# Performance work log

Hardware: AMD Instinct MI355X
Metric: run time of the kernel (lower is better)

## Reference

```python
import jax, jax.numpy as jnp
import numpy as np
from jax import lax

CHUNK = 256  # query chunk size (manual tiling block)

def setup_inputs() -> dict:
    key = jax.random.key(0)
    kq, kk, kv = jax.random.split(key, 3)
    shape = (2, 16, 2048, 128)  # [B, H, S, D]
    q = jax.random.normal(kq, shape, dtype=jnp.float32)
    k = jax.random.normal(kk, shape, dtype=jnp.float32)
    v = jax.random.normal(kv, shape, dtype=jnp.float32)
    return {"q": q, "k": k, "v": v}

def reference(q, k, v):
    # Chunked (memory-efficient) exact attention: softmax(QK^T/sqrt(D)) V,
    # computed one query block at a time so the full [S,S] score matrix
    # is never materialized.
    B, H, S, D = q.shape
    scale = jnp.asarray(1.0 / np.sqrt(D), dtype=q.dtype)
    n_chunks = S // CHUNK
    # [n_chunks, B, H, CHUNK, D]
    q_blocks = q.reshape(B, H, n_chunks, CHUNK, D).transpose(2, 0, 1, 3, 4)

    def step(carry, q_blk):
        # scores for this query block vs all keys: [B, H, CHUNK, S]
        s = jnp.einsum('bhqd,bhkd->bhqk', q_blk, k) * scale
        p = jax.nn.softmax(s, axis=-1)
        o = jnp.einsum('bhqk,bhkd->bhqd', p, v)
        return carry, o

    _, out_blocks = lax.scan(step, None, q_blocks)
    # [n_chunks, B, H, CHUNK, D] -> [B, H, S, D]
    out = out_blocks.transpose(1, 2, 0, 3, 4).reshape(B, H, S, D)
    return out
```

## Files before the change

kernel.cpp:

```cpp
#include <hip/hip_runtime.h>
#include <hip/hip_bf16.h>


typedef short short8 __attribute__((ext_vector_type(8)));
typedef float f32x4 __attribute__((ext_vector_type(4)));

#define MFMA16(a, b, c) __builtin_amdgcn_mfma_f32_16x16x32_bf16((a), (b), (c), 0, 0, 0)

#if __has_builtin(__builtin_amdgcn_exp2f)
#define EXP2(x) __builtin_amdgcn_exp2f(x)
#else
#define EXP2(x) exp2f(x)
#endif

constexpr int Dh  = 128;
constexpr int S_  = 2048;
constexpr int KVB = 64;
constexpr int NT  = S_ / KVB;
constexpr int WAVES = 8;
constexpr int QBLK  = 128;

__device__ __forceinline__ short f2bf(float f) {
    union { float f; unsigned u; } x; x.f = f;
    unsigned r = x.u + 0x7fffu + ((x.u >> 16) & 1u);
    return (short)(r >> 16);
}

__device__ __forceinline__ void gload16(const void* g, void* l) {
    __builtin_amdgcn_global_load_lds(
        (const __attribute__((address_space(1))) unsigned int*)g,
        (__attribute__((address_space(3))) unsigned int*)l, 16, 0, 0);
}

__global__ __launch_bounds__(256) void prep_k(const float* __restrict__ K,
                                              short* __restrict__ Kz) {
    int idx = blockIdx.x * 256 + threadIdx.x;
    int b   = idx & 15;
    int s   = (idx >> 4) & (S_ - 1);
    int sb  = b ^ (s & 15);
    const float* src = K + (size_t)(idx >> 4) * Dh + sb * 8;
    float4 f0 = ((const float4*)src)[0];
    float4 f1 = ((const float4*)src)[1];
    short8 o;
    o[0] = f2bf(f0.x); o[1] = f2bf(f0.y); o[2] = f2bf(f0.z); o[3] = f2bf(f0.w);
    o[4] = f2bf(f1.x); o[5] = f2bf(f1.y); o[6] = f2bf(f1.z); o[7] = f2bf(f1.w);
    *(short8*)(Kz + (size_t)idx * 8) = o;
}

__global__ __launch_bounds__(256) void prep_v(const float* __restrict__ V,
                                              short* __restrict__ Vt) {
    __shared__ short tr[64][72];
    int bid = blockIdx.x;
    int dg = bid & 1, seg = (bid >> 1) & 31, bh = bid >> 6;
    int t = threadIdx.x;
    int s = t >> 2, d0 = (t & 3) * 16;
    const float* src = V + (size_t)(bh * S_ + seg * 64 + s) * Dh + dg * 64 + d0;
    #pragma unroll
    for (int i = 0; i < 16; i += 4) {
        float4 f = *(const float4*)(src + i);
        tr[d0 + i + 0][s] = f2bf(f.x); tr[d0 + i + 1][s] = f2bf(f.y);
        tr[d0 + i + 2][s] = f2bf(f.z); tr[d0 + i + 3][s] = f2bf(f.w);
    }
    __syncthreads();
    int d = t >> 2, j0 = (t & 3) * 2;
    size_t ob = ((size_t)(bh * 32 + seg) * 128 + dg * 64 + d) * 64;
    #pragma unroll
    for (int jj = 0; jj < 2; ++jj) {
        int j = j0 + jj;
        int sj = (j ^ (d & 7)) * 8;
        short8 val = *(const short8*)&tr[d][sj];
        *(short8*)(Vt + ob + j * 8) = val;
    }
}

__global__ __launch_bounds__(512, 4)
void mea_fwd3(const float* __restrict__ Qg, const short* __restrict__ Kz,
              const short* __restrict__ Vt, float* __restrict__ Og, int nqt) {
    __shared__ __align__(16) short k0[KVB * Dh], k1[KVB * Dh];
    __shared__ __align__(16) short v0[Dh * KVB], v1[Dh * KVB];
    __shared__ __align__(16) short p_lds[WAVES][16][64];

    const int bid  = blockIdx.x;
    const int swz  = (bid & 7) * ((int)gridDim.x >> 3) + (bid >> 3);
    const int qt   = swz % nqt;
    const int bh   = swz / nqt;
    const int tid  = threadIdx.x;
    const int w    = tid >> 6;
    const int lane = tid & 63;
    const int lr   = lane & 15;
    const int lg   = lane >> 4;

    const size_t base  = (size_t)bh * S_ * Dh;
    const int    qrow0 = qt * QBLK + w * 16;
    const float  QSC = 0.08838834764831845f * 1.4426950408889634f;

    short8 qf[4];
    {
        const float* qp = Qg + base + (size_t)(qrow0 + lr) * Dh;
        #pragma unroll
        for (int kc = 0; kc < 4; ++kc) {
            const float4 f0 = *(const float4*)(qp + kc * 32 + lg * 8);
            const float4 f1 = *(const float4*)(qp + kc * 32 + lg * 8 + 4);
            short8 a;
            a[0] = f2bf(f0.x * QSC); a[1] = f2bf(f0.y * QSC);
            a[2] = f2bf(f0.z * QSC); a[3] = f2bf(f0.w * QSC);
            a[4] = f2bf(f1.x * QSC); a[5] = f2bf(f1.y * QSC);
            a[6] = f2bf(f1.z * QSC); a[7] = f2bf(f1.w * QSC);
            qf[kc] = a;
        }
    }

    f32x4 oacc[8];
    #pragma unroll
    for (int dt = 0; dt < 8; ++dt) oacc[dt] = (f32x4){0.f, 0.f, 0.f, 0.f};
    float mrun[4]  = {-1e30f, -1e30f, -1e30f, -1e30f};
    float lpart[4] = {0.f, 0.f, 0.f, 0.f};

    const short* ktile0 = Kz + (size_t)bh * S_ * Dh;
    const short* vtile0 = Vt + (size_t)bh * S_ * Dh;

    auto STAGE = [&](short* kl, short* vl, int t) {
        const short* kt = ktile0 + (size_t)t * (KVB * Dh);
        const short* vt = vtile0 + (size_t)t * (Dh * KVB);
        #pragma unroll
        for (int i = 0; i < 2; ++i) {
            const int o = (i * 8 + w) * 512;
            gload16(kt + o + lane * 8, kl + o);
            gload16(vt + o + lane * 8, vl + o);
        }
    };

    auto COMPUTE = [&](const short* kl, const short* vl) {
        f32x4 sac[4];
        #pragma unroll
        for (int ct = 0; ct < 4; ++ct) sac[ct] = (f32x4){0.f, 0.f, 0.f, 0.f};
        __builtin_amdgcn_s_setprio(1);
        #pragma unroll
        for (int kc = 0; kc < 4; ++kc) {
            #pragma unroll
            for (int ct = 0; ct < 4; ++ct) {
                const short8 b = *(const short8*)
                    &kl[(ct * 16 + lr) * Dh + (((kc * 4 + lg) ^ lr) * 8)];
                sac[ct] = MFMA16(qf[kc], b, sac[ct]);
            }
        }
        __builtin_amdgcn_s_setprio(0);

        float mxl[4];
        bool need = false;
        #pragma unroll
        for (int r = 0; r < 4; ++r) {
            mxl[r] = fmaxf(fmaxf(sac[0][r], sac[1][r]),
                           fmaxf(sac[2][r], sac[3][r]));
            need |= (mxl[r] > mrun[r] + 11.0f);
        }
        if (__any(need)) {
            #pragma unroll
            for (int r = 0; r < 4; ++r) {
                float m0 = mxl[r];
                #pragma unroll
                for (int mm = 1; mm < 16; mm <<= 1)
                    m0 = fmaxf(m0, __shfl_xor(m0, mm));
                float mnew = fmaxf(mrun[r], m0);
                float rc = EXP2(mrun[r] - mnew);
                mrun[r] = mnew;
                lpart[r] *= rc;
                #pragma unroll
                for (int dt = 0; dt < 8; ++dt) oacc[dt][r] *= rc;
            }
        }

        #pragma unroll
        for (int half = 0; half < 2; ++half) {
            #pragma unroll
            for (int r = 0; r < 4; ++r) {
                const int row = lg * 4 + r;
                float psum = 0.f;
                #pragma unroll
                for (int c2 = 0; c2 < 2; ++c2) {
                    const int ct = half * 2 + c2;
                    float p = EXP2(sac[ct][r] - mrun[r]);
                    psum += p;
                    p_lds[w][row][(((ct * 2 + (lr >> 3)) ^ (row & 7)) * 8) + (lr & 7)]
                        = f2bf(p);
                }
                lpart[r] += psum;
            }
            const short8 ap = *(const short8*)
                &p_lds[w][lr][((half * 4 + lg) ^ (lr & 7)) * 8];
            __builtin_amdgcn_s_setprio(1);
            #pragma unroll
            for (int dt = 0; dt < 8; ++dt) {
                const short8 bv = *(const short8*)
                    &vl[(dt * 16 + lr) * KVB + (((half * 4 + lg) ^ (lr & 7)) * 8)];
                oacc[dt] = MFMA16(ap, bv, oacc[dt]);
            }
            __builtin_amdgcn_s_setprio(0);
        }
    };

    STAGE(k0, v0, 0);
    __syncthreads();
    #pragma unroll 1
    for (int t = 0; t < NT; t += 2) {
        STAGE(k1, v1, t + 1);
        COMPUTE(k0, v0);
        __syncthreads();
        if (t + 2 < NT) STAGE(k0, v0, t + 2);
        COMPUTE(k1, v1);
        __syncthreads();
    }

    float linv[4];
    #pragma unroll
    for (int r = 0; r < 4; ++r) {
        float s = lpart[r];
        #pragma unroll
        for (int mm = 1; mm < 16; mm <<= 1) s += __shfl_xor(s, mm);
        linv[r] = 1.0f / s;
    }
    float* op = Og + base;
    #pragma unroll
    for (int dt = 0; dt < 8; ++dt)
        #pragma unroll
        for (int r = 0; r < 4; ++r)
            op[(size_t)(qrow0 + lg * 4 + r) * Dh + dt * 16 + lr]
                = oacc[dt][r] * linv[r];
}

constexpr int FKVB = 32;
constexpr int FKP  = 136;
constexpr int FVP  = 40;
constexpr int FPP  = 40;

__global__ __launch_bounds__(256, 2)
void mea_fwd_fb(const float* __restrict__ Qg, const float* __restrict__ Kg,
                const float* __restrict__ Vg, float* __restrict__ Og,
                int S, int nqt) {
    __shared__ __align__(16) short k_lds[FKVB][FKP];
    __shared__ __align__(16) short vT_lds[Dh][FVP];
    __shared__ __align__(16) short p_lds[4][16][FPP];

    const int qt = blockIdx.x % nqt;
    const int bh = blockIdx.x / nqt;
    const int tid = threadIdx.x;
    const int w = tid >> 6, lane = tid & 63;
    const int lr = lane & 15, lg = lane >> 4;
    const size_t base = (size_t)bh * S * Dh;
    const int qrow0 = qt * 64 + w * 16;
    const float scale = 0.08838834764831845f;

    short8 qf[4];
    {
        const float* qp = Qg + base + (size_t)(qrow0 + lr) * Dh;
        #pragma unroll
        for (int kc = 0; kc < 4; ++kc) {
            const float4 f0 = *(const float4*)(qp + kc * 32 + lg * 8);
            const float4 f1 = *(const float4*)(qp + kc * 32 + lg * 8 + 4);
            short8 a;
            a[0] = f2bf(f0.x); a[1] = f2bf(f0.y); a[2] = f2bf(f0.z); a[3] = f2bf(f0.w);
            a[4] = f2bf(f1.x); a[5] = f2bf(f1.y); a[6] = f2bf(f1.z); a[7] = f2bf(f1.w);
            qf[kc] = a;
        }
    }
    f32x4 oacc[8];
    #pragma unroll
    for (int dt = 0; dt < 8; ++dt) oacc[dt] = (f32x4){0.f, 0.f, 0.f, 0.f};
    float mrun[4] = {-1e30f, -1e30f, -1e30f, -1e30f};
    float lrun[4] = {0.f, 0.f, 0.f, 0.f};
    const int sr = tid >> 3, sc = (tid & 7) * 16;

    for (int kv0 = 0; kv0 < S; kv0 += FKVB) {
        {
            const float* kp = Kg + base + (size_t)(kv0 + sr) * Dh + sc;
            const float* vp = Vg + base + (size_t)(kv0 + sr) * Dh + sc;
            short8 pk0, pk1;
            float4 f0 = ((const float4*)kp)[0], f1 = ((const float4*)kp)[1];
            float4 f2 = ((const float4*)kp)[2], f3 = ((const float4*)kp)[3];
            pk0[0] = f2bf(f0.x); pk0[1] = f2bf(f0.y); pk0[2] = f2bf(f0.z); pk0[3] = f2bf(f0.w);
            pk0[4] = f2bf(f1.x); pk0[5] = f2bf(f1.y); pk0[6] = f2bf(f1.z); pk0[7] = f2bf(f1.w);
            pk1[0] = f2bf(f2.x); pk1[1] = f2bf(f2.y); pk1[2] = f2bf(f2.z); pk1[3] = f2bf(f2.w);
            pk1[4] = f2bf(f3.x); pk1[5] = f2bf(f3.y); pk1[6] = f2bf(f3.z); pk1[7] = f2bf(f3.w);
            *(short8*)&k_lds[sr][sc] = pk0;
            *(short8*)&k_lds[sr][sc + 8] = pk1;
            #pragma unroll
            for (int i = 0; i < 4; ++i) {
                float4 f = ((const float4*)vp)[i];
                vT_lds[sc + 4 * i + 0][sr] = f2bf(f.x);
                vT_lds[sc + 4 * i + 1][sr] = f2bf(f.y);
                vT_lds[sc + 4 * i + 2][sr] = f2bf(f.z);
                vT_lds[sc + 4 * i + 3][sr] = f2bf(f.w);
            }
        }
        __syncthreads();
        f32x4 s0 = (f32x4){0.f,0.f,0.f,0.f}, s1 = (f32x4){0.f,0.f,0.f,0.f};
        #pragma unroll
        for (int kc = 0; kc < 4; ++kc) {
            short8 b0 = *(const short8*)&k_lds[lr][kc * 32 + lg * 8];
            short8 b1 = *(const short8*)&k_lds[16 + lr][kc * 32 + lg * 8];
            s0 = MFMA16(qf[kc], b0, s0);
            s1 = MFMA16(qf[kc], b1, s1);
        }
        float resc[4];
        #pragma unroll
        for (int r = 0; r < 4; ++r) {
            float mxv = fmaxf(s0[r], s1[r]);
            #pragma unroll
            for (int m = 1; m < 16; m <<= 1) mxv = fmaxf(mxv, __shfl_xor(mxv, m));
            float mnew = fmaxf(mrun[r], mxv * scale);
            float rc = __expf(mrun[r] - mnew);
            mrun[r] = mnew;
            float p0 = __expf(s0[r] * scale - mnew);
            float p1 = __expf(s1[r] * scale - mnew);
            float rs = p0 + p1;
            #pragma unroll
            for (int m = 1; m < 16; m <<= 1) rs += __shfl_xor(rs, m);
            lrun[r] = lrun[r] * rc + rs;
            resc[r] = rc;
            p_lds[w][lg * 4 + r][lr] = f2bf(p0);
            p_lds[w][lg * 4 + r][16 + lr] = f2bf(p1);
        }
        #pragma unroll
        for (int dt = 0; dt < 8; ++dt) {
            f32x4 o = oacc[dt];
            o[0] *= resc[0]; o[1] *= resc[1]; o[2] *= resc[2]; o[3] *= resc[3];
            oacc[dt] = o;
        }
        short8 ap = *(const short8*)&p_lds[w][lr][lg * 8];
        #pragma unroll
        for (int dt = 0; dt < 8; ++dt) {
            short8 bv = *(const short8*)&vT_lds[dt * 16 + lr][lg * 8];
            oacc[dt] = MFMA16(ap, bv, oacc[dt]);
        }
        __syncthreads();
    }
    float inv[4];
    #pragma unroll
    for (int r = 0; r < 4; ++r) inv[r] = 1.0f / lrun[r];
    float* op = Og + base;
    #pragma unroll
    for (int dt = 0; dt < 8; ++dt)
        #pragma unroll
        for (int r = 0; r < 4; ++r)
            op[(size_t)(qrow0 + lg * 4 + r) * Dh + dt * 16 + lr] = oacc[dt][r] * inv[r];
}

extern "C" void kernel_launch(void* const* d_in, const int* in_sizes, int n_in,
                              void* d_out, int out_size, void* d_ws, size_t ws_size,
                              hipStream_t stream) {
    const float* q = (const float*)d_in[0];
    const float* k = (const float*)d_in[1];
    const float* v = (const float*)d_in[2];
    float* o = (float*)d_out;

    const int BH  = in_sizes[0] / (S_ * Dh);
    const int nqt = S_ / QBLK;

    const size_t kz_bytes = (size_t)BH * S_ * Dh * sizeof(short);
    const size_t need = 2 * kz_bytes;

    if (ws_size >= need) {
        short* Kz = (short*)d_ws;
        short* Vt = (short*)((char*)d_ws + kz_bytes);
        hipLaunchKernelGGL(prep_k, dim3(BH * S_ * 16 / 256), dim3(256), 0, stream, k, Kz);
        hipLaunchKernelGGL(prep_v, dim3(BH * (S_ / 64) * 2), dim3(256), 0, stream, v, Vt);
        hipLaunchKernelGGL(mea_fwd3, dim3(BH * nqt), dim3(512), 0, stream, q, Kz, Vt, o, nqt);
    } else {
        hipLaunchKernelGGL(mea_fwd_fb, dim3(BH * (S_ / 64)), dim3(256), 0, stream,
                           q, k, v, o, S_, S_ / 64);
    }
}
```

Before: 113.9 us.

## Switch attention kernel to 32x32 MFMA with transposed scores and register P exchange

Rewrites the main attention kernel to use 32x32x16 bf16 MFMA. It computes S^T (K as the A operand) so each lane owns one query row, which makes the row max and sum lane-local plus one cross-half shuffle. Probabilities are packed with v_cvt_pk_bf16_f32 and exchanged between lane halves via shuffles instead of going through LDS. Each block now covers 256 queries, so there are half as many blocks and K/V is reused more per block. The trade-off is more registers per thread (launch bounds drop to 2 blocks) and an LDS broadcast for the rescale factors.

Result: faster. 96.71 us (-15.1%).

```diff
diff --git a/kernel.cpp b/kernel.cpp
--- a/kernel.cpp
+++ b/kernel.cpp
@@ -3,9 +3,9 @@
 
 
 typedef short short8 __attribute__((ext_vector_type(8)));
-typedef float f32x4 __attribute__((ext_vector_type(4)));
-
-#define MFMA16(a, b, c) __builtin_amdgcn_mfma_f32_16x16x32_bf16((a), (b), (c), 0, 0, 0)
+typedef float f32x16 __attribute__((ext_vector_type(16)));
+
+#define MFMA32(a, b, c) __builtin_amdgcn_mfma_f32_32x32x16_bf16((a), (b), (c), 0, 0, 0)
 
 #if __has_builtin(__builtin_amdgcn_exp2f)
 #define EXP2(x) __builtin_amdgcn_exp2f(x)
@@ -18,12 +18,18 @@
 constexpr int KVB = 64;
 constexpr int NT  = S_ / KVB;
 constexpr int WAVES = 8;
-constexpr int QBLK  = 128;
+constexpr int QBLK  = 256;
 
 __device__ __forceinline__ short f2bf(float f) {
     union { float f; unsigned u; } x; x.f = f;
     unsigned r = x.u + 0x7fffu + ((x.u >> 16) & 1u);
     return (short)(r >> 16);
+}
+
+__device__ __forceinline__ unsigned pkbf(float lo, float hi) {
+    unsigned r;
+    asm("v_cvt_pk_bf16_f32 %0, %1, %2" : "=v"(r) : "v"(lo), "v"(hi));
+    return r;
 }
 
 __device__ __forceinline__ void gload16(const void* g, void* l) {
@@ -73,34 +79,36 @@
     }
 }
 
-__global__ __launch_bounds__(512, 4)
-void mea_fwd3(const float* __restrict__ Qg, const short* __restrict__ Kz,
+__global__ __launch_bounds__(512, 2)
+void mea_fwd4(const float* __restrict__ Qg, const short* __restrict__ Kz,
               const short* __restrict__ Vt, float* __restrict__ Og, int nqt) {
     __shared__ __align__(16) short k0[KVB * Dh], k1[KVB * Dh];
     __shared__ __align__(16) short v0[Dh * KVB], v1[Dh * KVB];
-    __shared__ __align__(16) short p_lds[WAVES][16][64];
-
-    const int bid  = blockIdx.x;
-    const int swz  = (bid & 7) * ((int)gridDim.x >> 3) + (bid >> 3);
-    const int qt   = swz % nqt;
-    const int bh   = swz / nqt;
+    __shared__ float bc_lds[WAVES][32];
+
+    const int bid = blockIdx.x;
+    const int cpx = (int)gridDim.x >> 3;
+    const int swz = (bid & 7) * cpx + (bid >> 3);
+    const int qt  = swz % nqt;
+    const int bh  = swz / nqt;
+
     const int tid  = threadIdx.x;
     const int w    = tid >> 6;
     const int lane = tid & 63;
-    const int lr   = lane & 15;
-    const int lg   = lane >> 4;
-
-    const size_t base  = (size_t)bh * S_ * Dh;
-    const int    qrow0 = qt * QBLK + w * 16;
-    const float  QSC = 0.08838834764831845f * 1.4426950408889634f;
-
-    short8 qf[4];
+    const int l31  = lane & 31;
+    const int hi   = lane >> 5;
+
+    const size_t base = (size_t)bh * S_ * Dh;
+    const int    qrow = qt * QBLK + w * 32 + l31;
+    const float  QSC  = 0.08838834764831845f * 1.4426950408889634f;
+
+    short8 qf[8];
     {
-        const float* qp = Qg + base + (size_t)(qrow0 + lr) * Dh;
-        #pragma unroll
-        for (int kc = 0; kc < 4; ++kc) {
-            const float4 f0 = *(const float4*)(qp + kc * 32 + lg * 8);
-            const float4 f1 = *(const float4*)(qp + kc * 32 + lg * 8 + 4);
+        const float* qp = Qg + base + (size_t)qrow * Dh;
+        #pragma unroll
+        for (int kc = 0; kc < 8; ++kc) {
+            const float4 f0 = *(const float4*)(qp + kc * 16 + hi * 8);
+            const float4 f1 = *(const float4*)(qp + kc * 16 + hi * 8 + 4);
             short8 a;
             a[0] = f2bf(f0.x * QSC); a[1] = f2bf(f0.y * QSC);
             a[2] = f2bf(f0.z * QSC); a[3] = f2bf(f0.w * QSC);
@@ -110,93 +118,109 @@
         }
     }
 
-    f32x4 oacc[8];
-    #pragma unroll
-    for (int dt = 0; dt < 8; ++dt) oacc[dt] = (f32x4){0.f, 0.f, 0.f, 0.f};
-    float mrun[4]  = {-1e30f, -1e30f, -1e30f, -1e30f};
-    float lpart[4] = {0.f, 0.f, 0.f, 0.f};
-
-    const short* ktile0 = Kz + (size_t)bh * S_ * Dh;
-    const short* vtile0 = Vt + (size_t)bh * S_ * Dh;
+    f32x16 oacc[4];
+    #pragma unroll
+    for (int dt = 0; dt < 4; ++dt)
+        #pragma unroll
+        for (int r = 0; r < 16; ++r) oacc[dt][r] = 0.f;
+    float mrun = -1e30f, lpart = 0.f;
+
+    const short* kt0 = Kz + base;
+    const short* vt0 = Vt + base;
 
     auto STAGE = [&](short* kl, short* vl, int t) {
-        const short* kt = ktile0 + (size_t)t * (KVB * Dh);
-        const short* vt = vtile0 + (size_t)t * (Dh * KVB);
+        const short* ks = kt0 + (size_t)t * (KVB * Dh);
+        const short* vs = vt0 + (size_t)t * (Dh * KVB);
         #pragma unroll
         for (int i = 0; i < 2; ++i) {
-            const int o = (i * 8 + w) * 512;
-            gload16(kt + o + lane * 8, kl + o);
-            gload16(vt + o + lane * 8, vl + o);
+            const int ou = (i * 8 + w) * 512;
+            gload16(ks + ou + lane * 8, kl + ou);
+            gload16(vs + ou + lane * 8, vl + ou);
         }
     };
 
     auto COMPUTE = [&](const short* kl, const short* vl) {
-        f32x4 sac[4];
-        #pragma unroll
-        for (int ct = 0; ct < 4; ++ct) sac[ct] = (f32x4){0.f, 0.f, 0.f, 0.f};
+        f32x16 sa, sb;
+        #pragma unroll
+        for (int r = 0; r < 16; ++r) { sa[r] = 0.f; sb[r] = 0.f; }
         __builtin_amdgcn_s_setprio(1);
         #pragma unroll
-        for (int kc = 0; kc < 4; ++kc) {
-            #pragma unroll
-            for (int ct = 0; ct < 4; ++ct) {
-                const short8 b = *(const short8*)
-                    &kl[(ct * 16 + lr) * Dh + (((kc * 4 + lg) ^ lr) * 8)];
-                sac[ct] = MFMA16(qf[kc], b, sac[ct]);
+        for (int kc = 0; kc < 8; ++kc) {
+            const int go = (((kc * 2 + hi) ^ (l31 & 15)) * 8);
+            const short8 a0 = *(const short8*)&kl[l31 * Dh + go];
+            const short8 a1 = *(const short8*)&kl[(32 + l31) * Dh + go];
+            sa = MFMA32(a0, qf[kc], sa);
+            sb = MFMA32(a1, qf[kc], sb);
+        }
+        __builtin_amdgcn_s_setprio(0);
+
+        float mxl = sa[0];
+        #pragma unroll
+        for (int r = 1; r < 16; ++r) mxl = fmaxf(mxl, sa[r]);
+        #pragma unroll
+        for (int r = 0; r < 16; ++r) mxl = fmaxf(mxl, sb[r]);
+        if (__any(mxl > mrun + 8.0f)) {
+            float mo   = fmaxf(mxl, __shfl_xor(mxl, 32));
+            float mnew = fmaxf(mrun, mo);
+            float rc   = EXP2(mrun - mnew);
+            mrun = mnew;
+            lpart *= rc;
+            if (!hi) bc_lds[w][l31] = rc;
+            #pragma unroll
+            for (int m = 0; m < 4; ++m) {
+                const float4 rcv = *(const float4*)&bc_lds[w][m * 8 + 4 * hi];
+                #pragma unroll
+                for (int t2 = 0; t2 < 4; ++t2) {
+                    const float f = (&rcv.x)[t2];
+                    #pragma unroll
+                    for (int dt = 0; dt < 4; ++dt) oacc[dt][m * 4 + t2] *= f;
+                }
             }
         }
+
+        f32x16 pa, pb;
+        float s0 = 0.f, s1 = 0.f;
+        #pragma unroll
+        for (int r = 0; r < 16; ++r) { pa[r] = EXP2(sa[r] - mrun); s0 += pa[r]; }
+        #pragma unroll
+        for (int r = 0; r < 16; ++r) { pb[r] = EXP2(sb[r] - mrun); s1 += pb[r]; }
+        lpart += s0 + s1;
+
+        short8 pf[4];
+        #pragma unroll
+        for (int ks = 0; ks < 4; ++ks) {
+            const int qA = (ks & 1) * 2, qB = qA + 1;
+            float eA0, eA1, eA2, eA3, eB0, eB1, eB2, eB3;
+            if (ks < 2) {
+                eA0 = pa[qA*4+0]; eA1 = pa[qA*4+1]; eA2 = pa[qA*4+2]; eA3 = pa[qA*4+3];
+                eB0 = pa[qB*4+0]; eB1 = pa[qB*4+1]; eB2 = pa[qB*4+2]; eB3 = pa[qB*4+3];
+            } else {
+                eA0 = pb[qA*4+0]; eA1 = pb[qA*4+1]; eA2 = pb[qA*4+2]; eA3 = pb[qA*4+3];
+                eB0 = pb[qB*4+0]; eB1 = pb[qB*4+1]; eB2 = pb[qB*4+2]; eB3 = pb[qB*4+3];
+            }
+            const unsigned uA0 = pkbf(eA0, eA1), uA1 = pkbf(eA2, eA3);
+            const unsigned uB0 = pkbf(eB0, eB1), uB1 = pkbf(eB2, eB3);
+            const unsigned y0 = hi ? uA0 : uB0;
+            const unsigned y1 = hi ? uA1 : uB1;
+            const unsigned r0 = (unsigned)__shfl_xor((int)y0, 32);
+            const unsigned r1 = (unsigned)__shfl_xor((int)y1, 32);
+            unsigned wd[4];
+            wd[0] = hi ? r0 : uA0;  wd[1] = hi ? r1 : uA1;
+            wd[2] = hi ? uB0 : r0;  wd[3] = hi ? uB1 : r1;
+            pf[ks] = *(const short8*)wd;
+        }
+
+        __builtin_amdgcn_s_setprio(1);
+        #pragma unroll
+        for (int dt = 0; dt < 4; ++dt) {
+            #pragma unroll
+            for (int ks = 0; ks < 4; ++ks) {
+                const short8 bv = *(const short8*)
+                    &vl[(dt * 32 + l31) * KVB + (((ks * 2 + hi) ^ (l31 & 7)) * 8)];
+                oacc[dt] = MFMA32(pf[ks], bv, oacc[dt]);
+            }
+        }
         __builtin_amdgcn_s_setprio(0);
-
-        float mxl[4];
-        bool need = false;
-        #pragma unroll
-        for (int r = 0; r < 4; ++r) {
-            mxl[r] = fmaxf(fmaxf(sac[0][r], sac[1][r]),
-                           fmaxf(sac[2][r], sac[3][r]));
-            need |= (mxl[r] > mrun[r] + 11.0f);
-        }
-        if (__any(need)) {
-            #pragma unroll
-            for (int r = 0; r < 4; ++r) {
-                float m0 = mxl[r];
-                #pragma unroll
-                for (int mm = 1; mm < 16; mm <<= 1)
-                    m0 = fmaxf(m0, __shfl_xor(m0, mm));
-                float mnew = fmaxf(mrun[r], m0);
-                float rc = EXP2(mrun[r] - mnew);
-                mrun[r] = mnew;
-                lpart[r] *= rc;
-                #pragma unroll
-                for (int dt = 0; dt < 8; ++dt) oacc[dt][r] *= rc;
-            }
-        }
-
-        #pragma unroll
-        for (int half = 0; half < 2; ++half) {
-            #pragma unroll
-            for (int r = 0; r < 4; ++r) {
-                const int row = lg * 4 + r;
-                float psum = 0.f;
-                #pragma unroll
-                for (int c2 = 0; c2 < 2; ++c2) {
-                    const int ct = half * 2 + c2;
-                    float p = EXP2(sac[ct][r] - mrun[r]);
-                    psum += p;
-                    p_lds[w][row][(((ct * 2 + (lr >> 3)) ^ (row & 7)) * 8) + (lr & 7)]
-                        = f2bf(p);
-                }
-                lpart[r] += psum;
-            }
-            const short8 ap = *(const short8*)
-                &p_lds[w][lr][((half * 4 + lg) ^ (lr & 7)) * 8];
-            __builtin_amdgcn_s_setprio(1);
-            #pragma unroll
-            for (int dt = 0; dt < 8; ++dt) {
-                const short8 bv = *(const short8*)
-                    &vl[(dt * 16 + lr) * KVB + (((half * 4 + lg) ^ (lr & 7)) * 8)];
-                oacc[dt] = MFMA16(ap, bv, oacc[dt]);
-            }
-            __builtin_amdgcn_s_setprio(0);
-        }
     };
 
     STAGE(k0, v0, 0);
@@ -211,23 +235,28 @@
         __syncthreads();
     }
 
-    float linv[4];
-    #pragma unroll
-    for (int r = 0; r < 4; ++r) {
-        float s = lpart[r];
-        #pragma unroll
-        for (int mm = 1; mm < 16; mm <<= 1) s += __shfl_xor(s, mm);
-        linv[r] = 1.0f / s;
+    {
+        const float tot = lpart + __shfl_xor(lpart, 32);
+        if (!hi) bc_lds[w][l31] = 1.0f / tot;
     }
     float* op = Og + base;
     #pragma unroll
-    for (int dt = 0; dt < 8; ++dt)
-        #pragma unroll
-        for (int r = 0; r < 4; ++r)
-            op[(size_t)(qrow0 + lg * 4 + r) * Dh + dt * 16 + lr]
-                = oacc[dt][r] * linv[r];
-}
-
+    for (int m = 0; m < 4; ++m) {
+        const float4 li = *(const float4*)&bc_lds[w][m * 8 + 4 * hi];
+        #pragma unroll
+        for (int t2 = 0; t2 < 4; ++t2) {
+            const int row  = m * 8 + 4 * hi + t2;
+            const float lf = (&li.x)[t2];
+            #pragma unroll
+            for (int dt = 0; dt < 4; ++dt)
+                op[(size_t)(qt * QBLK + w * 32 + row) * Dh + dt * 32 + l31]
+                    = oacc[dt][m * 4 + t2] * lf;
+        }
+    }
+}
+
+typedef float f32x4 __attribute__((ext_vector_type(4)));
+#define MFMA16(a, b, c) __builtin_amdgcn_mfma_f32_16x16x32_bf16((a), (b), (c), 0, 0, 0)
 constexpr int FKVB = 32;
 constexpr int FKP  = 136;
 constexpr int FVP  = 40;
@@ -364,7 +393,7 @@
         short* Vt = (short*)((char*)d_ws + kz_bytes);
         hipLaunchKernelGGL(prep_k, dim3(BH * S_ * 16 / 256), dim3(256), 0, stream, k, Kz);
         hipLaunchKernelGGL(prep_v, dim3(BH * (S_ / 64) * 2), dim3(256), 0, stream, v, Vt);
-        hipLaunchKernelGGL(mea_fwd3, dim3(BH * nqt), dim3(512), 0, stream, q, Kz, Vt, o, nqt);
+        hipLaunchKernelGGL(mea_fwd4, dim3(BH * nqt), dim3(512), 0, stream, q, Kz, Vt, o, nqt);
     } else {
         hipLaunchKernelGGL(mea_fwd_fb, dim3(BH * (S_ / 64)), dim3(256), 0, stream,
                            q, k, v, o, S_, S_ / 64);
```
